# Kernel optimization log

Hardware: AMD Instinct MI355X
Metric: run time of the kernel (lower is better)

The kernel has to match this reference:

```python
import jax, jax.numpy as jnp
import numpy as np

ATOM_DIM, HID, N_LAYERS, N_HEADS, PF_DIM = 34, 256, 2, 8, 1024
B, NA, NP = 32, 512, 1024


def setup_inputs() -> dict:
    key = jax.random.key(0)
    ks = iter(jax.random.split(key, 32))
    def rn(shape, s=0.02):
        return jax.random.normal(next(ks), shape, dtype=jnp.float32) * s
    L = N_LAYERS
    z = lambda *s: jnp.zeros(s, jnp.float32)
    return {
        "trg": jax.random.normal(next(ks), (B, NA, ATOM_DIM), dtype=jnp.float32),
        "src": jax.random.normal(next(ks), (B, NP, HID), dtype=jnp.float32),
        "ft_w": rn((HID, ATOM_DIM)), "ft_b": z(HID),
        "ln_g": jnp.ones((L, HID), jnp.float32), "ln_b": z(L, HID),
        "sa_wq": rn((L, HID, HID)), "sa_bq": z(L, HID),
        "sa_wk": rn((L, HID, HID)), "sa_bk": z(L, HID),
        "sa_wv": rn((L, HID, HID)), "sa_bv": z(L, HID),
        "sa_wf": rn((L, HID, HID)), "sa_bf": z(L, HID),
        "ea_wq": rn((L, HID, HID)), "ea_bq": z(L, HID),
        "ea_wk": rn((L, HID, HID)), "ea_bk": z(L, HID),
        "ea_wv": rn((L, HID, HID)), "ea_bv": z(L, HID),
        "ea_wf": rn((L, HID, HID)), "ea_bf": z(L, HID),
        "pf_w1": rn((L, PF_DIM, HID)), "pf_b1": z(L, PF_DIM),
        "pf_w2": rn((L, HID, PF_DIM)), "pf_b2": z(L, HID),
        "fc1_w": rn((256, HID)), "fc1_b": z(256),
        "fc2_w": rn((2, 256)), "fc2_b": z(2),
    }


def _ln(x, g, b, eps=1e-5):
    m = jnp.mean(x, axis=-1, keepdims=True)
    v = jnp.mean(jnp.square(x - m), axis=-1, keepdims=True)
    return (x - m) * jax.lax.rsqrt(v + eps) * g + b


def _attn(xq, xkv, wq, bq, wk, bk, wv, bv, wf, bf):
    b_, lq, h = xq.shape
    d = h // N_HEADS
    q = (xq @ wq.T + bq).reshape(b_, lq, N_HEADS, d).transpose(0, 2, 1, 3)
    k = (xkv @ wk.T + bk).reshape(b_, -1, N_HEADS, d).transpose(0, 2, 1, 3)
    v = (xkv @ wv.T + bv).reshape(b_, -1, N_HEADS, d).transpose(0, 2, 1, 3)
    scale = jnp.sqrt(jnp.float32(d))  # TransformerCPI: sqrt(hid_dim // n_heads)
    a = jax.nn.softmax(jnp.einsum('bhqd,bhkd->bhqk', q, k) / scale, axis=-1)
    o = jnp.einsum('bhqk,bhkd->bhqd', a, v).transpose(0, 2, 1, 3).reshape(b_, lq, h)
    return o @ wf.T + bf


def reference(trg, src, ft_w, ft_b, ln_g, ln_b,
              sa_wq, sa_bq, sa_wk, sa_bk, sa_wv, sa_bv, sa_wf, sa_bf,
              ea_wq, ea_bq, ea_wk, ea_bk, ea_wv, ea_bv, ea_wf, ea_bf,
              pf_w1, pf_b1, pf_w2, pf_b2, fc1_w, fc1_b, fc2_w, fc2_b):
    x = trg @ ft_w.T + ft_b  # [B, NA, HID]
    for l in range(N_LAYERS):
        x = _ln(x + _attn(x, x, sa_wq[l], sa_bq[l], sa_wk[l], sa_bk[l],
                          sa_wv[l], sa_bv[l], sa_wf[l], sa_bf[l]), ln_g[l], ln_b[l])
        x = _ln(x + _attn(x, src, ea_wq[l], ea_bq[l], ea_wk[l], ea_bk[l],
                          ea_wv[l], ea_bv[l], ea_wf[l], ea_bf[l]), ln_g[l], ln_b[l])
        h = jax.nn.relu(x @ pf_w1[l].T + pf_b1[l]) @ pf_w2[l].T + pf_b2[l]
        x = _ln(x + h, ln_g[l], ln_b[l])
    # norm-weighted attention pooling (replaces the nested Python loops)
    w = jax.nn.softmax(jnp.linalg.norm(x, axis=2), axis=1)  # [B, NA]
    pooled = jnp.einsum('bn,bnh->bh', w, x)  # [B, HID]
    return jax.nn.relu(pooled @ fc1_w.T + fc1_b) @ fc2_w.T + fc2_b
```

## Files before the change

kernel.cpp:

```cpp
#include <hip/hip_runtime.h>
#include <hip/hip_bf16.h>
#include <math.h>

#define B_   32
#define NA   512
#define NP   1024
#define HID  256
#define NH   8
#define DH   32
#define PF   1024

typedef short bf16x8 __attribute__((ext_vector_type(8)));
typedef float f32x4  __attribute__((ext_vector_type(4)));
typedef float f32x16 __attribute__((ext_vector_type(16)));
typedef unsigned u32x4 __attribute__((ext_vector_type(4)));

#define ZERO16 {0.f,0.f,0.f,0.f,0.f,0.f,0.f,0.f,0.f,0.f,0.f,0.f,0.f,0.f,0.f,0.f}

static __device__ inline unsigned short f2bf(float f) {
    __hip_bfloat16 h = __float2bfloat16(f);
    unsigned short u;
    __builtin_memcpy(&u, &h, 2);
    return u;
}
static __device__ inline float bf2f(unsigned short u) {
    unsigned x = ((unsigned)u) << 16;
    return __uint_as_float(x);
}
static __device__ inline unsigned cvtpk(float lo, float hi) {
    return (unsigned)f2bf(lo) | ((unsigned)f2bf(hi) << 16);
}
static __device__ inline bf16x8 pack8(float4 a, float4 b) {
    bf16x8 r;
    r[0] = (short)f2bf(a.x); r[1] = (short)f2bf(a.y);
    r[2] = (short)f2bf(a.z); r[3] = (short)f2bf(a.w);
    r[4] = (short)f2bf(b.x); r[5] = (short)f2bf(b.y);
    r[6] = (short)f2bf(b.z); r[7] = (short)f2bf(b.w);
    return r;
}
static __device__ inline void gload16(const unsigned short* g, unsigned short* l) {
    __builtin_amdgcn_global_load_lds(
        (const __attribute__((address_space(1))) void*)g,
        (__attribute__((address_space(3))) void*)l, 16, 0, 0);
}

__global__ __launch_bounds__(256) void ft_kernel(const float* __restrict__ trg,
    const float* __restrict__ w, const float* __restrict__ b,
    float* __restrict__ out, unsigned short* __restrict__ outb)
{
    __shared__ float Ws[256][35];
    int tid = threadIdx.x;
    for (int k = 0; k < 34; ++k) Ws[tid][k] = w[tid*34 + k];
    float bias = b[tid];
    __syncthreads();
    int m0 = blockIdx.x * 32;
    for (int r = 0; r < 32; ++r) {
        int m = m0 + r;
        const float* tr = trg + (size_t)m*34;
        float acc = bias;
        #pragma unroll
        for (int k = 0; k < 34; ++k) acc += tr[k] * Ws[tid][k];
        out [(size_t)m*HID + tid] = acc;
        outb[(size_t)m*HID + tid] = f2bf(acc);
    }
}

__global__ __launch_bounds__(256) void cvt_bf16(const float* __restrict__ in,
    unsigned short* __restrict__ outb, int n8)
{
    int i = blockIdx.x*256 + threadIdx.x;
    int stride = gridDim.x*256;
    for (; i < n8; i += stride) {
        float4 a = *(const float4*)(in + (size_t)i*8);
        float4 b = *(const float4*)(in + (size_t)i*8 + 4);
        *(bf16x8*)(outb + (size_t)i*8) = pack8(a, b);
    }
}

__global__ __launch_bounds__(256) void cvt_w(
    const float* __restrict__ s0, const float* __restrict__ s1,
    const float* __restrict__ s2, const float* __restrict__ s3,
    const float* __restrict__ s4, const float* __restrict__ s5,
    const float* __restrict__ s6, const float* __restrict__ s7,
    const float* __restrict__ s8, const float* __restrict__ s9,
    unsigned short* __restrict__ dst)
{
    const int z = blockIdx.z;
    const float* src;
    switch (z) {
        case 0: src = s0; break; case 1: src = s1; break;
        case 2: src = s2; break; case 3: src = s3; break;
        case 4: src = s4; break; case 5: src = s5; break;
        case 6: src = s6; break; case 7: src = s7; break;
        case 8: src = s8; break; default: src = s9; break;
    }
    const int n8 = (z < 8) ? 16384 : 65536;
    const size_t off = (z < 8) ? (size_t)z*131072 : (1048576u + (size_t)(z-8)*524288);
    unsigned short* o = dst + off;
    int i = blockIdx.x*256 + threadIdx.x;
    const int stride = gridDim.x*256;
    for (; i < n8; i += stride) {
        float4 a = *(const float4*)(src + (size_t)i*8);
        float4 b = *(const float4*)(src + (size_t)i*8 + 4);
        *(bf16x8*)(o + (size_t)i*8) = pack8(a, b);
    }
}

static __device__ inline void gemm_core(const unsigned short* __restrict__ Ab,
    const unsigned short* __restrict__ Wb, const float* __restrict__ bias,
    void* __restrict__ Cv, int M, int N, int K, int mode, int L, float oscale,
    int bx, int by)
{
    __shared__ __attribute__((aligned(16))) unsigned short As[2][128*64];
    __shared__ __attribute__((aligned(16))) unsigned short Ws[2][64*64];
    const int tid = threadIdx.x;
    const int wave = tid >> 6, lane = tid & 63, lq = lane & 15, g = lane >> 4;
    const int wr = wave >> 1, wc = wave & 1;
    const int m0 = by * 128, n0 = bx * 64;

    const int srow = lane >> 3;
    const int scol = ((lane & 7) ^ ((lane >> 3) & 7)) * 8;
    const int cswz = (lq & 7) * 8;

    f32x4 acc[4][2] = {};

    auto STAGE = [&](int kt, int buf) {
        const int k0 = kt * 64;
        #pragma unroll
        for (int c = 0; c < 4; ++c) {
            const int row = wave*32 + c*8;
            gload16(Ab + (size_t)(m0 + row + srow)*K + k0 + scol,
                    &As[buf][row*64]);
        }
        #pragma unroll
        for (int c = 0; c < 2; ++c) {
            const int row = wave*16 + c*8;
            gload16(Wb + (size_t)(n0 + row + srow)*K + k0 + scol,
                    &Ws[buf][row*64]);
        }
    };

    const int nk = K / 64;
    STAGE(0, 0);
    __syncthreads();
    for (int kt = 0; kt < nk; ++kt) {
        const int cur = kt & 1;
        if (kt + 1 < nk) STAGE(kt + 1, cur ^ 1);
        const unsigned short* Ac = &As[cur][0];
        const unsigned short* Wc = &Ws[cur][0];
        #pragma unroll
        for (int ks = 0; ks < 2; ++ks) {
            const int co = (ks*32 + g*8) ^ cswz;
            bf16x8 bf0 = *(const bf16x8*)&Wc[(wc*32 +  0 + lq)*64 + co];
            bf16x8 bf1 = *(const bf16x8*)&Wc[(wc*32 + 16 + lq)*64 + co];
            #pragma unroll
            for (int i = 0; i < 4; ++i) {
                bf16x8 af = *(const bf16x8*)&Ac[(wr*64 + i*16 + lq)*64 + co];
                acc[i][0] = __builtin_amdgcn_mfma_f32_16x16x32_bf16(af, bf0, acc[i][0], 0, 0, 0);
                acc[i][1] = __builtin_amdgcn_mfma_f32_16x16x32_bf16(af, bf1, acc[i][1], 0, 0, 0);
            }
        }
        __syncthreads();
    }

    float bb[2];
    #pragma unroll
    for (int j = 0; j < 2; ++j) bb[j] = bias[n0 + wc*32 + j*16 + lq];

    #pragma unroll
    for (int i = 0; i < 4; ++i) {
        const int mb = m0 + wr*64 + i*16 + 4*g;
        #pragma unroll
        for (int j = 0; j < 2; ++j) {
            const int n = n0 + wc*32 + j*16 + lq;
            f32x4 v = acc[i][j];
            #pragma unroll
            for (int r = 0; r < 4; ++r) v[r] = (v[r] + bb[j]) * oscale;
            if (mode == 0) {
                float* Cf = (float*)Cv;
                #pragma unroll
                for (int r = 0; r < 4; ++r) Cf[(size_t)(mb + r)*N + n] = v[r];
            } else if (mode == 1) {
                unsigned short* Cb = (unsigned short*)Cv;
                #pragma unroll
                for (int r = 0; r < 4; ++r) Cb[(size_t)(mb + r)*N + n] = f2bf(v[r]);
            } else if (mode == 3) {
                unsigned short* Cb = (unsigned short*)Cv;
                #pragma unroll
                for (int r = 0; r < 4; ++r) Cb[(size_t)(mb + r)*N + n] = f2bf(fmaxf(v[r], 0.f));
            } else if (mode == 4) {
                unsigned short* Cb = (unsigned short*)Cv;
                const int bI = mb / L, kk = mb % L;
                const int hh = n >> 5, d = n & 31;
                const int t2 = kk >> 5, dc = d >> 4, hi2 = (d >> 3) & 1;
                unsigned short* base = Cb
                    + ((size_t)(((bI*NH + hh)*(L >> 5) + t2)*2 + dc))*512
                    + ((kk & 31) + 32*hi2)*8 + (d & 7);
                base[0]  = f2bf(v[0]); base[8]  = f2bf(v[1]);
                base[16] = f2bf(v[2]); base[24] = f2bf(v[3]);
            } else {
                unsigned short* Cb = (unsigned short*)Cv;
                const int bI = mb / L, kk = mb % L;
                const int hh = n >> 5, d = n & 31;
                const int t = kk >> 6, oct = (kk >> 3) & 7;
                const int c = oct >> 1, hiV = oct & 1;
                ushort4 pk;
                pk.x = f2bf(v[0]); pk.y = f2bf(v[1]); pk.z = f2bf(v[2]); pk.w = f2bf(v[3]);
                *(ushort4*)(Cb
                    + ((size_t)(((bI*NH + hh)*(L >> 6) + t)*4 + c))*512
                    + (d + 32*hiV)*8 + (kk & 7)) = pk;
            }
        }
    }
}

static __device__ inline void xcd_swz(int d, int nx, int nxy, int& bx, int& by)
{
    const int w = (d & 7) * (nxy >> 3) + (d >> 3);
    bx = w % nx; by = w / nx;
}

__global__ __launch_bounds__(256) void gemm_mfma(const unsigned short* __restrict__ A,
    const unsigned short* __restrict__ W, const float* __restrict__ bias,
    void* __restrict__ C, int M, int N, int K, int mode, int L)
{
    int bx, by;
    xcd_swz(blockIdx.y*gridDim.x + blockIdx.x, gridDim.x, gridDim.x*gridDim.y, bx, by);
    gemm_core(A, W, bias, C, M, N, K, mode, L, 1.f, bx, by);
}

__global__ __launch_bounds__(256) void qkv_mfma(const unsigned short* __restrict__ Aq,
    const unsigned short* __restrict__ Akv,
    const unsigned short* __restrict__ Wq, const float* __restrict__ bq,
    const unsigned short* __restrict__ Wk, const float* __restrict__ bk,
    const unsigned short* __restrict__ Wv, const float* __restrict__ bv,
    void* __restrict__ qo, void* __restrict__ ko, void* __restrict__ vo,
    int Mq, int Mkv, int L)
{
    const int z = blockIdx.z;
    const unsigned short* A = (z == 0) ? Aq : Akv;
    const unsigned short* W = (z == 0) ? Wq : ((z == 1) ? Wk : Wv);
    const float* bb = (z == 0) ? bq : ((z == 1) ? bk : bv);
    void* C = (z == 0) ? qo : ((z == 1) ? ko : vo);
    const int M = (z == 0) ? Mq : Mkv;
    const int mode = (z == 0) ? 1 : ((z == 1) ? 4 : 5);
    const float sc = (z == 0) ? 0.25504082364238727f : 1.f;
    int bx, by;
    xcd_swz(blockIdx.y*gridDim.x + blockIdx.x, gridDim.x, gridDim.x*gridDim.y, bx, by);
    if (by * 128 >= M) return;
    gemm_core(A, W, bb, C, M, HID, HID, mode, L, sc, bx, by);
}

__global__ __launch_bounds__(256) void attn_mfma(const unsigned short* __restrict__ Qb,
    const unsigned short* __restrict__ KF, const unsigned short* __restrict__ VF,
    unsigned short* __restrict__ O, int Lk)
{
    __shared__ float Ll[4][32];
    const int orig = blockIdx.x;
    const int sw = (orig & 7) * 128 + (orig >> 3);
    const int qt = sw & 3;
    const int h  = (sw >> 2) & 7;
    const int b  = sw >> 5;
    const int tid = threadIdx.x, w = tid >> 6, lane = tid & 63;
    const int q32 = lane & 31, hi = lane >> 5;

    const unsigned short* qp = Qb + ((size_t)(b*NA + qt*128 + w*32 + q32))*HID + h*DH + hi*8;
    bf16x8 qf0 = *(const bf16x8*)qp;
    bf16x8 qf1 = *(const bf16x8*)(qp + 16);

    const unsigned short* Kf = KF + (size_t)((b*NH + h)*(Lk >> 5)*2)*512 + lane*8;
    const unsigned short* Vf = VF + (size_t)((b*NH + h)*(Lk >> 6)*4)*512 + lane*8;

    f32x16 o_acc = ZERO16;
    float lacc = 0.f;

    bf16x8 kfA[4], kfB[4], vfT[4];
    auto LOADK = [&](int t, bf16x8* kd) {
        #pragma unroll
        for (int f = 0; f < 4; ++f)
            kd[f] = *(const bf16x8*)(Kf + (size_t)(t*4 + f)*512);
    };
    auto STEP = [&](const bf16x8* kf, int t) {
        #pragma unroll
        for (int c = 0; c < 4; ++c)
            vfT[c] = *(const bf16x8*)(Vf + (size_t)(t*4 + c)*512);
        f32x16 st0 = ZERO16, st1 = ZERO16;
        st0 = __builtin_amdgcn_mfma_f32_32x32x16_bf16(kf[0], qf0, st0, 0, 0, 0);
        st0 = __builtin_amdgcn_mfma_f32_32x32x16_bf16(kf[1], qf1, st0, 0, 0, 0);
        st1 = __builtin_amdgcn_mfma_f32_32x32x16_bf16(kf[2], qf0, st1, 0, 0, 0);
        st1 = __builtin_amdgcn_mfma_f32_32x32x16_bf16(kf[3], qf1, st1, 0, 0, 0);
        bf16x8 pa[4];
        float lp = 0.f;
        #pragma unroll
        for (int c = 0; c < 4; ++c) {
            const f32x16& s = (c < 2) ? st0 : st1;
            const int rb = (c & 1) * 8;
            float p0 = __builtin_amdgcn_exp2f(s[rb+0]);
            float p1 = __builtin_amdgcn_exp2f(s[rb+1]);
            float p2 = __builtin_amdgcn_exp2f(s[rb+2]);
            float p3 = __builtin_amdgcn_exp2f(s[rb+3]);
            float p4 = __builtin_amdgcn_exp2f(s[rb+4]);
            float p5 = __builtin_amdgcn_exp2f(s[rb+5]);
            float p6 = __builtin_amdgcn_exp2f(s[rb+6]);
            float p7 = __builtin_amdgcn_exp2f(s[rb+7]);
            lp += (p0+p1) + (p2+p3) + (p4+p5) + (p6+p7);
            unsigned A1 = cvtpk(p0, p1), A2 = cvtpk(p2, p3);
            unsigned B1 = cvtpk(p4, p5), B2 = cvtpk(p6, p7);
            auto r1 = __builtin_amdgcn_permlane32_swap(A1, B1, false, false);
            auto r2 = __builtin_amdgcn_permlane32_swap(A2, B2, false, false);
            u32x4 pw; pw[0] = r1[0]; pw[1] = r2[0]; pw[2] = r1[1]; pw[3] = r2[1];
            __builtin_memcpy(&pa[c], &pw, 16);
        }
        lacc += lp;
        #pragma unroll
        for (int c = 0; c < 4; ++c)
            o_acc = __builtin_amdgcn_mfma_f32_32x32x16_bf16(pa[c], vfT[c], o_acc, 0, 0, 0);
    };

    const int nt = Lk >> 6;
    LOADK(0, kfA);
    for (int t = 0; t < nt; t += 2) {
        LOADK(t + 1, kfB);
        STEP(kfA, t);
        if (t + 2 < nt) LOADK(t + 2, kfA);
        STEP(kfB, t + 1);
    }

    float lt = lacc + __shfl_xor(lacc, 32);
    float linv = 1.f / lt;
    if (hi == 0) Ll[w][q32] = linv;
    f32x4 li[4];
    #pragma unroll
    for (int jg = 0; jg < 4; ++jg) li[jg] = *(const f32x4*)&Ll[w][jg*8 + hi*4];

    unsigned short* Op = O + ((size_t)(b*NA + qt*128 + w*32))*HID + h*DH + q32;
    #pragma unroll
    for (int jg = 0; jg < 4; ++jg) {
        #pragma unroll
        for (int r2 = 0; r2 < 4; ++r2) {
            const int q = jg*8 + hi*4 + r2;
            Op[(size_t)q*HID] = f2bf(o_acc[jg*4 + r2] * li[jg][r2]);
        }
    }
}

__global__ __launch_bounds__(256) void add_ln(float* __restrict__ x,
    const unsigned short* __restrict__ t, const float* __restrict__ g,
    const float* __restrict__ bt, unsigned short* __restrict__ xb)
{
    const int row = blockIdx.x*4 + (threadIdx.x >> 6);
    const int lane = threadIdx.x & 63;
    const size_t base = (size_t)row*HID + lane*4;
    float4 v = *(const float4*)(x + base);
    ushort4 tu = *(const ushort4*)(t + base);
    v.x += bf2f(tu.x); v.y += bf2f(tu.y); v.z += bf2f(tu.z); v.w += bf2f(tu.w);
    float s = v.x + v.y + v.z + v.w;
    #pragma unroll
    for (int o = 32; o > 0; o >>= 1) s += __shfl_xor(s, o);
    float mean = s * (1.f/256.f);
    float4 d = {v.x - mean, v.y - mean, v.z - mean, v.w - mean};
    float q2 = d.x*d.x + d.y*d.y + d.z*d.z + d.w*d.w;
    #pragma unroll
    for (int o = 32; o > 0; o >>= 1) q2 += __shfl_xor(q2, o);
    float rs = rsqrtf(q2*(1.f/256.f) + 1e-5f);
    float4 gv = *(const float4*)(g + lane*4);
    float4 bv = *(const float4*)(bt + lane*4);
    float4 ov;
    ov.x = d.x*rs*gv.x + bv.x; ov.y = d.y*rs*gv.y + bv.y;
    ov.z = d.z*rs*gv.z + bv.z; ov.w = d.w*rs*gv.w + bv.w;
    *(float4*)(x + base) = ov;
    ushort4 pk;
    pk.x = f2bf(ov.x); pk.y = f2bf(ov.y); pk.z = f2bf(ov.z); pk.w = f2bf(ov.w);
    *(ushort4*)(xb + base) = pk;
}

__global__ __launch_bounds__(256) void norms_k(const float* __restrict__ x,
    float* __restrict__ nw)
{
    const int row = blockIdx.x*4 + (threadIdx.x >> 6);
    const int lane = threadIdx.x & 63;
    float4 v = *(const float4*)(x + (size_t)row*HID + lane*4);
    float s = v.x*v.x + v.y*v.y + v.z*v.z + v.w*v.w;
    #pragma unroll
    for (int o = 32; o > 0; o >>= 1) s += __shfl_xor(s, o);
    if (lane == 0) nw[row] = sqrtf(s);
}

__global__ __launch_bounds__(256) void pooled_k(const float* __restrict__ x,
    const float* __restrict__ nw, float* __restrict__ pooled)
{
    __shared__ float sw[NA];
    __shared__ float red[256];
    __shared__ float part[8][33];
    const int b = blockIdx.x, hc = blockIdx.y;
    const int tid = threadIdx.x;
    const float* nb = nw + (size_t)b*NA;
    float v0 = nb[tid], v1 = nb[tid + 256];
    red[tid] = fmaxf(v0, v1); __syncthreads();
    for (int s = 128; s > 0; s >>= 1) { if (tid < s) red[tid] = fmaxf(red[tid], red[tid+s]); __syncthreads(); }
    float mx = red[0]; __syncthreads();
    float e0 = __expf(v0 - mx), e1 = __expf(v1 - mx);
    sw[tid] = e0; sw[tid + 256] = e1;
    red[tid] = e0 + e1; __syncthreads();
    for (int s = 128; s > 0; s >>= 1) { if (tid < s) red[tid] += red[tid+s]; __syncthreads(); }
    float inv = 1.f / red[0];
    __syncthreads();
    const int ng = tid >> 5, col = tid & 31;
    const float* xp = x + (size_t)b*NA*HID + hc*32 + col;
    float acc = 0.f;
    for (int n = ng; n < NA; n += 8)
        acc += sw[n] * xp[(size_t)n*HID];
    part[ng][col] = acc;
    __syncthreads();
    if (tid < 32) {
        float s = 0.f;
        #pragma unroll
        for (int i = 0; i < 8; ++i) s += part[i][tid];
        pooled[(size_t)b*HID + hc*32 + tid] = s * inv;
    }
}

__global__ __launch_bounds__(256) void head_k(const float* __restrict__ pooled,
    const float* __restrict__ fc1w, const float* __restrict__ fc1b,
    const float* __restrict__ fc2w, const float* __restrict__ fc2b,
    float* __restrict__ out)
{
    __shared__ float p[HID];
    __shared__ float a1[HID];
    const int b = blockIdx.x, tid = threadIdx.x;
    p[tid] = pooled[(size_t)b*HID + tid];
    __syncthreads();
    float s1 = fc1b[tid];
    const float* w1 = fc1w + (size_t)tid*HID;
    for (int k2 = 0; k2 < HID; k2 += 4) {
        float4 w = *(const float4*)(w1 + k2);
        s1 += p[k2]*w.x + p[k2+1]*w.y + p[k2+2]*w.z + p[k2+3]*w.w;
    }
    a1[tid] = fmaxf(s1, 0.f);
    __syncthreads();
    if (tid < 2) {
        float s2 = fc2b[tid];
        const float* w2 = fc2w + (size_t)tid*HID;
        for (int k2 = 0; k2 < HID; ++k2) s2 += a1[k2] * w2[k2];
        out[b*2 + tid] = s2;
    }
}

extern "C" void kernel_launch(void* const* d_in, const int* in_sizes, int n_in,
                              void* d_out, int out_size, void* d_ws, size_t ws_size,
                              hipStream_t stream)
{
    const float* trg  = (const float*)d_in[0];
    const float* src  = (const float*)d_in[1];
    const float* ft_w = (const float*)d_in[2];
    const float* ft_b = (const float*)d_in[3];
    const float* ln_g = (const float*)d_in[4];
    const float* ln_b = (const float*)d_in[5];
    const float* sa_wq = (const float*)d_in[6];  const float* sa_bq = (const float*)d_in[7];
    const float* sa_wk = (const float*)d_in[8];  const float* sa_bk = (const float*)d_in[9];
    const float* sa_wv = (const float*)d_in[10]; const float* sa_bv = (const float*)d_in[11];
    const float* sa_wf = (const float*)d_in[12]; const float* sa_bf = (const float*)d_in[13];
    const float* ea_wq = (const float*)d_in[14]; const float* ea_bq = (const float*)d_in[15];
    const float* ea_wk = (const float*)d_in[16]; const float* ea_bk = (const float*)d_in[17];
    const float* ea_wv = (const float*)d_in[18]; const float* ea_bv = (const float*)d_in[19];
    const float* ea_wf = (const float*)d_in[20]; const float* ea_bf = (const float*)d_in[21];
    const float* pf_w1 = (const float*)d_in[22]; const float* pf_b1 = (const float*)d_in[23];
    const float* pf_w2 = (const float*)d_in[24]; const float* pf_b2 = (const float*)d_in[25];
    const float* fc1w  = (const float*)d_in[26]; const float* fc1b  = (const float*)d_in[27];
    const float* fc2w  = (const float*)d_in[28]; const float* fc2b  = (const float*)d_in[29];
    float* out = (float*)d_out;

    const size_t NTOK = (size_t)B_*NA;
    const size_t NSRC = (size_t)B_*NP;
    float* ws = (float*)d_ws;
    float* x  = ws;
    float* nw = x + NTOK*HID;
    float* pooled = nw + NTOK;
    unsigned short* ub   = (unsigned short*)(pooled + B_*HID);
    unsigned short* xb   = ub + NTOK*HID;
    unsigned short* tb   = xb + NTOK*HID;
    unsigned short* srcb = tb + NTOK*HID;
    unsigned short* qb   = srcb + NSRC*HID;
    unsigned short* kb   = qb + NTOK*HID;
    unsigned short* vTb  = kb + NSRC*HID;
    unsigned short* wb   = vTb + NSRC*HID;
    unsigned short* hb   = qb;

    unsigned short* saq_b = wb;
    unsigned short* sak_b = wb +  131072;
    unsigned short* sav_b = wb +  262144;
    unsigned short* saf_b = wb +  393216;
    unsigned short* eaq_b = wb +  524288;
    unsigned short* eak_b = wb +  655360;
    unsigned short* eav_b = wb +  786432;
    unsigned short* eaf_b = wb +  917504;
    unsigned short* pw1_b = wb + 1048576;
    unsigned short* pw2_b = wb + 1572864;

    const int M = (int)NTOK;
    dim3 blk(256);

    cvt_w<<<dim3(64, 1, 10), blk, 0, stream>>>(sa_wq, sa_wk, sa_wv, sa_wf,
        ea_wq, ea_wk, ea_wv, ea_wf, pf_w1, pf_w2, wb);
    ft_kernel<<<M/32, blk, 0, stream>>>(trg, ft_w, ft_b, x, xb);
    cvt_bf16<<<1024, blk, 0, stream>>>(src, srcb, (int)(NSRC*HID/8));

    for (int l = 0; l < 2; ++l) {
        const size_t wo = (size_t)l*HID*HID, bo = (size_t)l*HID;
        qkv_mfma<<<dim3(HID/64, M/128, 3), blk, 0, stream>>>(xb, xb,
            saq_b+wo, sa_bq+bo, sak_b+wo, sa_bk+bo, sav_b+wo, sa_bv+bo,
            qb, kb, vTb, M, M, NA);
        attn_mfma<<<dim3(1024), blk, 0, stream>>>(qb, kb, vTb, tb, NA);
        gemm_mfma<<<dim3(HID/64, M/128), blk, 0, stream>>>(tb, saf_b+wo, sa_bf+bo, ub, M, HID, HID, 1, 0);
        add_ln<<<M/4, blk, 0, stream>>>(x, ub, ln_g+bo, ln_b+bo, xb);
        qkv_mfma<<<dim3(HID/64, (int)NSRC/128, 3), blk, 0, stream>>>(xb, srcb,
            eaq_b+wo, ea_bq+bo, eak_b+wo, ea_bk+bo, eav_b+wo, ea_bv+bo,
            qb, kb, vTb, M, (int)NSRC, NP);
        attn_mfma<<<dim3(1024), blk, 0, stream>>>(qb, kb, vTb, tb, NP);
        gemm_mfma<<<dim3(HID/64, M/128), blk, 0, stream>>>(tb, eaf_b+wo, ea_bf+bo, ub, M, HID, HID, 1, 0);
        add_ln<<<M/4, blk, 0, stream>>>(x, ub, ln_g+bo, ln_b+bo, xb);
        gemm_mfma<<<dim3(PF/64, M/128), blk, 0, stream>>>(xb, pw1_b+(size_t)l*PF*HID, pf_b1+(size_t)l*PF, hb, M, PF, HID, 3, 0);
        gemm_mfma<<<dim3(HID/64, M/128), blk, 0, stream>>>(hb, pw2_b+(size_t)l*HID*PF, pf_b2+bo, ub, M, HID, PF, 1, 0);
        add_ln<<<M/4, blk, 0, stream>>>(x, ub, ln_g+bo, ln_b+bo, xb);
    }

    norms_k<<<M/4, blk, 0, stream>>>(x, nw);
    pooled_k<<<dim3(B_, 8), blk, 0, stream>>>(x, nw, pooled);
    head_k<<<B_, blk, 0, stream>>>(pooled, fc1w, fc1b, fc2w, fc2b, out);
}
```

Before: 443.1 us.

## Fuse output-projection GEMMs with residual add and LayerNorm, fold norms into last

Introduces a gemm_ln kernel in which each 512-thread block computes a full 64-row by 256-column tile, so it holds complete rows and can apply the bias, residual add and LayerNorm in its epilogue through a shared-memory staging buffer. This replaces the separate gemm_mfma plus add_ln pairs for the attention output projections and the FFN second GEMM, and the final layer also writes row norms, which removes norms_k. It is meant to save the bf16 intermediate round trip through global memory and several kernel launches. In exchange, the grid is much smaller (256 blocks) and uses a large shared-memory footprint, which can lower occupancy and parallelism.

```diff
diff --git a/kernel.cpp b/kernel.cpp
--- a/kernel.cpp
+++ b/kernel.cpp
@@ -176,11 +176,7 @@
             f32x4 v = acc[i][j];
             #pragma unroll
             for (int r = 0; r < 4; ++r) v[r] = (v[r] + bb[j]) * oscale;
-            if (mode == 0) {
-                float* Cf = (float*)Cv;
-                #pragma unroll
-                for (int r = 0; r < 4; ++r) Cf[(size_t)(mb + r)*N + n] = v[r];
-            } else if (mode == 1) {
+            if (mode == 1) {
                 unsigned short* Cb = (unsigned short*)Cv;
                 #pragma unroll
                 for (int r = 0; r < 4; ++r) Cb[(size_t)(mb + r)*N + n] = f2bf(v[r]);
@@ -251,6 +247,111 @@
     gemm_core(A, W, bb, C, M, HID, HID, mode, L, sc, bx, by);
 }
 
+__global__ __launch_bounds__(512) void gemm_ln(const unsigned short* __restrict__ Ab,
+    const unsigned short* __restrict__ Wb, const float* __restrict__ bias,
+    const float* __restrict__ lng, const float* __restrict__ lnb,
+    float* __restrict__ x, unsigned short* __restrict__ xb,
+    float* __restrict__ nrm, int K)
+{
+    __shared__ __attribute__((aligned(16))) char smem[81920];
+    unsigned short* As0 = (unsigned short*)smem;
+    unsigned short* Ws0 = (unsigned short*)(smem + 16384);
+    float* ys = (float*)smem;
+    const int tid = threadIdx.x;
+    const int w = tid >> 6, lane = tid & 63, lq = lane & 15, g = lane >> 4;
+    const int wc2 = w & 3, wh = w >> 2;
+    const int m0 = blockIdx.x * 64;
+
+    const int srow = lane >> 3;
+    const int scol = ((lane & 7) ^ srow) * 8;
+    const int cswz = (lq & 7) * 8;
+
+    f32x4 acc[4][2] = {};
+
+    auto STAGE = [&](int kt, int buf) {
+        const int k0 = kt * 64;
+        {   const int row = w * 8;
+            gload16(Ab + (size_t)(m0 + row + srow)*K + k0 + scol,
+                    As0 + buf*4096 + row*64);
+        }
+        #pragma unroll
+        for (int c = 0; c < 4; ++c) {
+            const int row = w*32 + c*8;
+            gload16(Wb + (size_t)(row + srow)*K + k0 + scol,
+                    Ws0 + buf*16384 + row*64);
+        }
+    };
+
+    const int nk = K / 64;
+    STAGE(0, 0);
+    __syncthreads();
+    for (int kt = 0; kt < nk; ++kt) {
+        const int cur = kt & 1;
+        if (kt + 1 < nk) STAGE(kt + 1, cur ^ 1);
+        const unsigned short* Ac = As0 + cur*4096;
+        const unsigned short* Wc = Ws0 + cur*16384;
+        #pragma unroll
+        for (int ks = 0; ks < 2; ++ks) {
+            const int co = (ks*32 + g*8) ^ cswz;
+            bf16x8 bf0 = *(const bf16x8*)&Wc[(wc2*64 + wh*32 +  0 + lq)*64 + co];
+            bf16x8 bf1 = *(const bf16x8*)&Wc[(wc2*64 + wh*32 + 16 + lq)*64 + co];
+            #pragma unroll
+            for (int i = 0; i < 4; ++i) {
+                bf16x8 af = *(const bf16x8*)&Ac[(i*16 + lq)*64 + co];
+                acc[i][0] = __builtin_amdgcn_mfma_f32_16x16x32_bf16(af, bf0, acc[i][0], 0, 0, 0);
+                acc[i][1] = __builtin_amdgcn_mfma_f32_16x16x32_bf16(af, bf1, acc[i][1], 0, 0, 0);
+            }
+        }
+        __syncthreads();
+    }
+
+    float bb0 = bias[wc2*64 + wh*32 +  0 + lq];
+    float bb1 = bias[wc2*64 + wh*32 + 16 + lq];
+    #pragma unroll
+    for (int i = 0; i < 4; ++i) {
+        const int col0 = wc2*64 + wh*32 + lq;
+        #pragma unroll
+        for (int r = 0; r < 4; ++r) {
+            const int row = i*16 + 4*g + r;
+            ys[row*260 + col0]      = acc[i][0][r] + bb0;
+            ys[row*260 + col0 + 16] = acc[i][1][r] + bb1;
+        }
+    }
+    __syncthreads();
+
+    float4 gv = *(const float4*)(lng + lane*4);
+    float4 bv = *(const float4*)(lnb + lane*4);
+    for (int it = 0; it < 8; ++it) {
+        const int row = w*8 + it;
+        const size_t gbase = (size_t)(m0 + row)*HID + lane*4;
+        float4 y = *(float4*)&ys[row*260 + lane*4];
+        float4 xv = *(const float4*)(x + gbase);
+        y.x += xv.x; y.y += xv.y; y.z += xv.z; y.w += xv.w;
+        float s = y.x + y.y + y.z + y.w;
+        #pragma unroll
+        for (int o = 32; o > 0; o >>= 1) s += __shfl_xor(s, o);
+        float mean = s * (1.f/256.f);
+        float4 d = {y.x - mean, y.y - mean, y.z - mean, y.w - mean};
+        float q2 = d.x*d.x + d.y*d.y + d.z*d.z + d.w*d.w;
+        #pragma unroll
+        for (int o = 32; o > 0; o >>= 1) q2 += __shfl_xor(q2, o);
+        float rs = rsqrtf(q2*(1.f/256.f) + 1e-5f);
+        float4 ov;
+        ov.x = d.x*rs*gv.x + bv.x; ov.y = d.y*rs*gv.y + bv.y;
+        ov.z = d.z*rs*gv.z + bv.z; ov.w = d.w*rs*gv.w + bv.w;
+        *(float4*)(x + gbase) = ov;
+        ushort4 pk;
+        pk.x = f2bf(ov.x); pk.y = f2bf(ov.y); pk.z = f2bf(ov.z); pk.w = f2bf(ov.w);
+        *(ushort4*)(xb + gbase) = pk;
+        if (nrm) {
+            float q3 = ov.x*ov.x + ov.y*ov.y + ov.z*ov.z + ov.w*ov.w;
+            #pragma unroll
+            for (int o = 32; o > 0; o >>= 1) q3 += __shfl_xor(q3, o);
+            if (lane == 0) nrm[m0 + row] = sqrtf(q3);
+        }
+    }
+}
+
 __global__ __launch_bounds__(256) void attn_mfma(const unsigned short* __restrict__ Qb,
     const unsigned short* __restrict__ KF, const unsigned short* __restrict__ VF,
     unsigned short* __restrict__ O, int Lk)
@@ -342,48 +443,6 @@
             Op[(size_t)q*HID] = f2bf(o_acc[jg*4 + r2] * li[jg][r2]);
         }
     }
-}
-
-__global__ __launch_bounds__(256) void add_ln(float* __restrict__ x,
-    const unsigned short* __restrict__ t, const float* __restrict__ g,
-    const float* __restrict__ bt, unsigned short* __restrict__ xb)
-{
-    const int row = blockIdx.x*4 + (threadIdx.x >> 6);
-    const int lane = threadIdx.x & 63;
-    const size_t base = (size_t)row*HID + lane*4;
-    float4 v = *(const float4*)(x + base);
-    ushort4 tu = *(const ushort4*)(t + base);
-    v.x += bf2f(tu.x); v.y += bf2f(tu.y); v.z += bf2f(tu.z); v.w += bf2f(tu.w);
-    float s = v.x + v.y + v.z + v.w;
-    #pragma unroll
-    for (int o = 32; o > 0; o >>= 1) s += __shfl_xor(s, o);
-    float mean = s * (1.f/256.f);
-    float4 d = {v.x - mean, v.y - mean, v.z - mean, v.w - mean};
-    float q2 = d.x*d.x + d.y*d.y + d.z*d.z + d.w*d.w;
-    #pragma unroll
-    for (int o = 32; o > 0; o >>= 1) q2 += __shfl_xor(q2, o);
-    float rs = rsqrtf(q2*(1.f/256.f) + 1e-5f);
-    float4 gv = *(const float4*)(g + lane*4);
-    float4 bv = *(const float4*)(bt + lane*4);
-    float4 ov;
-    ov.x = d.x*rs*gv.x + bv.x; ov.y = d.y*rs*gv.y + bv.y;
-    ov.z = d.z*rs*gv.z + bv.z; ov.w = d.w*rs*gv.w + bv.w;
-    *(float4*)(x + base) = ov;
-    ushort4 pk;
-    pk.x = f2bf(ov.x); pk.y = f2bf(ov.y); pk.z = f2bf(ov.z); pk.w = f2bf(ov.w);
-    *(ushort4*)(xb + base) = pk;
-}
-
-__global__ __launch_bounds__(256) void norms_k(const float* __restrict__ x,
-    float* __restrict__ nw)
-{
-    const int row = blockIdx.x*4 + (threadIdx.x >> 6);
-    const int lane = threadIdx.x & 63;
-    float4 v = *(const float4*)(x + (size_t)row*HID + lane*4);
-    float s = v.x*v.x + v.y*v.y + v.z*v.z + v.w*v.w;
-    #pragma unroll
-    for (int o = 32; o > 0; o >>= 1) s += __shfl_xor(s, o);
-    if (lane == 0) nw[row] = sqrtf(s);
 }
 
 __global__ __launch_bounds__(256) void pooled_k(const float* __restrict__ x,
@@ -476,8 +535,7 @@
     float* x  = ws;
     float* nw = x + NTOK*HID;
     float* pooled = nw + NTOK;
-    unsigned short* ub   = (unsigned short*)(pooled + B_*HID);
-    unsigned short* xb   = ub + NTOK*HID;
+    unsigned short* xb   = (unsigned short*)(pooled + B_*HID);
     unsigned short* tb   = xb + NTOK*HID;
     unsigned short* srcb = tb + NTOK*HID;
     unsigned short* qb   = srcb + NSRC*HID;
@@ -511,20 +569,19 @@
             saq_b+wo, sa_bq+bo, sak_b+wo, sa_bk+bo, sav_b+wo, sa_bv+bo,
             qb, kb, vTb, M, M, NA);
         attn_mfma<<<dim3(1024), blk, 0, stream>>>(qb, kb, vTb, tb, NA);
-        gemm_mfma<<<dim3(HID/64, M/128), blk, 0, stream>>>(tb, saf_b+wo, sa_bf+bo, ub, M, HID, HID, 1, 0);
-        add_ln<<<M/4, blk, 0, stream>>>(x, ub, ln_g+bo, ln_b+bo, xb);
+        gemm_ln<<<dim3(M/64), dim3(512), 0, stream>>>(tb, saf_b+wo, sa_bf+bo,
+            ln_g+bo, ln_b+bo, x, xb, nullptr, HID);
         qkv_mfma<<<dim3(HID/64, (int)NSRC/128, 3), blk, 0, stream>>>(xb, srcb,
             eaq_b+wo, ea_bq+bo, eak_b+wo, ea_bk+bo, eav_b+wo, ea_bv+bo,
             qb, kb, vTb, M, (int)NSRC, NP);
         attn_mfma<<<dim3(1024), blk, 0, stream>>>(qb, kb, vTb, tb, NP);
-        gemm_mfma<<<dim3(HID/64, M/128), blk, 0, stream>>>(tb, eaf_b+wo, ea_bf+bo, ub, M, HID, HID, 1, 0);
-        add_ln<<<M/4, blk, 0, stream>>>(x, ub, ln_g+bo, ln_b+bo, xb);
+        gemm_ln<<<dim3(M/64), dim3(512), 0, stream>>>(tb, eaf_b+wo, ea_bf+bo,
+            ln_g+bo, ln_b+bo, x, xb, nullptr, HID);
         gemm_mfma<<<dim3(PF/64, M/128), blk, 0, stream>>>(xb, pw1_b+(size_t)l*PF*HID, pf_b1+(size_t)l*PF, hb, M, PF, HID, 3, 0);
-        gemm_mfma<<<dim3(HID/64, M/128), blk, 0, stream>>>(hb, pw2_b+(size_t)l*HID*PF, pf_b2+bo, ub, M, HID, PF, 1, 0);
-        add_ln<<<M/4, blk, 0, stream>>>(x, ub, ln_g+bo, ln_b+bo, xb);
-    }
-
-    norms_k<<<M/4, blk, 0, stream>>>(x, nw);
+        gemm_ln<<<dim3(M/64), dim3(512), 0, stream>>>(hb, pw2_b+(size_t)l*HID*PF, pf_b2+bo,
+            ln_g+bo, ln_b+bo, x, xb, (l == 1) ? nw : nullptr, PF);
+    }
+
     pooled_k<<<dim3(B_, 8), blk, 0, stream>>>(x, nw, pooled);
     head_k<<<B_, blk, 0, stream>>>(pooled, fc1w, fc1b, fc2w, fc2b, out);
 }
```

New measurement: 417.3 us, median of 2. 5.8% less time.
